# Kernel optimization log

Measured on AMD Instinct MI355X. Metric: run time of the kernel, lower is better.

Reference implementation:

```python
import jax, jax.numpy as jnp
import numpy as np
import math

V, E, N, L, S_BLOCK, R = 50257, 1024, 16, 8, 1024, 4
B, S = 2, 1024
H = E // N
IPAD = 0


def layer_norm(x, w, b, eps=1e-5):
    mu = jnp.mean(x, axis=-1, keepdims=True)
    var = jnp.mean(jnp.square(x - mu), axis=-1, keepdims=True)
    return (x - mu) * jax.lax.rsqrt(var + eps) * w + b


def setup_inputs():
    key = jax.random.key(0)
    ks = jax.random.split(key, 10)
    nrm = lambda k, shape: jax.random.normal(k, shape, jnp.float32) * 0.02
    return {
        "x": jax.random.randint(ks[0], (B, S), 1, V, dtype=jnp.int32),
        "tok_emb": nrm(ks[1], (V, E)),
        "pos_emb": nrm(ks[2], (S_BLOCK, E)),
        "dec_ln_w": jnp.ones((E,), jnp.float32),
        "dec_ln_b": jnp.zeros((E,), jnp.float32),
        "qkv_w": nrm(ks[3], (L, 3 * E, E)),
        "qkv_b": jnp.zeros((L, 3 * E), jnp.float32),
        "attn_proj_w": nrm(ks[4], (L, E, E)),
        "attn_proj_b": jnp.zeros((L, E), jnp.float32),
        "ln1_w": jnp.ones((L, E), jnp.float32),
        "ln1_b": jnp.zeros((L, E), jnp.float32),
        "fc_w": nrm(ks[5], (L, R * E, E)),
        "fc_b": jnp.zeros((L, R * E), jnp.float32),
        "mlp_proj_w": nrm(ks[6], (L, E, R * E)),
        "mlp_proj_b": jnp.zeros((L, E), jnp.float32),
        "ln2_w": jnp.ones((L, E), jnp.float32),
        "ln2_b": jnp.zeros((L, E), jnp.float32),
        "fin_ln_w": jnp.ones((E,), jnp.float32),
        "fin_ln_b": jnp.zeros((E,), jnp.float32),
    }


def _forward(x, tok_emb, pos_emb, dec_ln_w, dec_ln_b, qkv_w, qkv_b,
             attn_proj_w, attn_proj_b, ln1_w, ln1_b, fc_w, fc_b,
             mlp_proj_w, mlp_proj_b, ln2_w, ln2_b, fin_ln_w, fin_ln_b):
    # token + positional embedding
    h = tok_emb[x] + pos_emb[:S][None, :, :]  # [B,S,E]
    # attention mask: causal AND key-not-pad (ipad=0, no cache -> C=0)
    causal = jnp.tril(jnp.ones((S, S), bool))  # [S,S]
    keypad = (x != IPAD)  # [B,S]
    mask = causal[None, None, :, :] & keypad[:, None, None, :]  # [B,1,S,S]
    scale = 1.0 / math.sqrt(H)

    # Decoder: ln then dropout(eval no-op) before blocks
    h = layer_norm(h, dec_ln_w, dec_ln_b)

    def block(h, p):
        (qw, qb, pw, pb, l1w, l1b, fw, fb, mw, mb, l2w, l2b) = p
        qkv = h @ qw.T + qb  # [B,S,3E]
        q, k, v = jnp.split(qkv, 3, axis=-1)
        q = q.reshape(B, S, N, H).transpose(0, 2, 1, 3)  # [B,N,S,H]
        k = k.reshape(B, S, N, H).transpose(0, 2, 1, 3)
        v = v.reshape(B, S, N, H).transpose(0, 2, 1, 3)
        scores = jnp.einsum('bnsh,bnth->bnst', q, k) * scale  # [B,N,S,S]
        scores = jnp.where(mask, scores, -jnp.inf)
        attn = jax.nn.softmax(scores, axis=-1)
        o = jnp.einsum('bnst,bnth->bnsh', attn, v)
        o = o.transpose(0, 2, 1, 3).reshape(B, S, E)
        o = o @ pw.T + pb
        h = layer_norm(o + h, l1w, l1b)  # post-norm
        m = jax.nn.gelu(h @ fw.T + fb, approximate=False) @ mw.T + mb
        h = layer_norm(m + h, l2w, l2b)
        return h, None

    params = (qkv_w, qkv_b, attn_proj_w, attn_proj_b, ln1_w, ln1_b,
              fc_w, fc_b, mlp_proj_w, mlp_proj_b, ln2_w, ln2_b)
    h, _ = jax.lax.scan(block, h, params)
    # final Transformer LayerNorm
    return layer_norm(h, fin_ln_w, fin_ln_b)


def reference(x, tok_emb, pos_emb, dec_ln_w, dec_ln_b, qkv_w, qkv_b,
              attn_proj_w, attn_proj_b, ln1_w, ln1_b, fc_w, fc_b,
              mlp_proj_w, mlp_proj_b, ln2_w, ln2_b, fin_ln_w, fin_ln_b):
    return _forward(x, tok_emb, pos_emb, dec_ln_w, dec_ln_b, qkv_w, qkv_b,
                    attn_proj_w, attn_proj_b, ln1_w, ln1_b, fc_w, fc_b,
                    mlp_proj_w, mlp_proj_b, ln2_w, ln2_b, fin_ln_w, fin_ln_b)
```

## Files before the change

kernel.cpp:

```cpp
#include <hip/hip_runtime.h>
#include <hip/hip_bf16.h>

#define E 1024
#define SLEN 1024
#define QKV3 3072
#define HD 64

typedef unsigned short u16;
typedef unsigned int   u32;
typedef __bf16 bf16x8 __attribute__((ext_vector_type(8)));
typedef float  f32x4  __attribute__((ext_vector_type(4)));
typedef float  fv4    __attribute__((ext_vector_type(4)));
typedef u32    uv2    __attribute__((ext_vector_type(2)));

__device__ __forceinline__ u16 f2bf(float f) {
  __hip_bfloat16 h = __float2bfloat16(f);
  return __builtin_bit_cast(u16, h);
}
__device__ __forceinline__ u32 pk2(float a, float b) {
  return (u32)f2bf(a) | ((u32)f2bf(b) << 16);
}
__device__ __forceinline__ float bf2f(u32 lo16) {
  const u32 b = lo16 << 16;
  return __builtin_bit_cast(float, b);
}

__device__ __forceinline__ void gload16(const u16* g, u16* l) {
  __builtin_amdgcn_global_load_lds(
      (const __attribute__((address_space(1))) void*)g,
      (__attribute__((address_space(3))) void*)l, 16, 0, 0);
}

__device__ __forceinline__ int swzP(int row, int ch) { return (row<<4) + (ch ^ (row & 7)); }

__global__ __launch_bounds__(256)
void f2b4(const float* __restrict__ s0, u16* __restrict__ d0, int n0,
          const float* __restrict__ s1, u16* __restrict__ d1, int n1,
          const float* __restrict__ s2, u16* __restrict__ d2, int n2,
          const float* __restrict__ s3, u16* __restrict__ d3, int n3)
{
  const int total = n0 + n1 + n2 + n3;
  const int stride = gridDim.x * 256;
  for (int i = blockIdx.x * 256 + threadIdx.x; i < total; i += stride) {
    const float* s; u16* d; int j = i;
    if (j < n0) { s = s0; d = d0; }
    else if ((j -= n0) < n1) { s = s1; d = d1; }
    else if ((j -= n1) < n2) { s = s2; d = d2; }
    else { j -= n2; s = s3; d = d3; }
    const fv4 v = __builtin_nontemporal_load((const fv4*)s + j);
    uv2 o; o.x = pk2(v.x, v.y); o.y = pk2(v.z, v.w);
    ((uv2*)d)[j] = o;
  }
}

template<int BN, int OUTBF, int GELU, int SK, int SWCX, int SWCY>
__global__ __launch_bounds__(256)
void gemm_lds(const u16* __restrict__ A, const u16* __restrict__ W,
              const float* __restrict__ bias, void* __restrict__ Cv,
              int M, int N, int K)
{
  static_assert(!(GELU && SK > 1), "gelu needs full sum");
  constexpr int BM = 128;
  __shared__ __align__(16) u16 sA[3][BM*32];
  __shared__ __align__(16) u16 sB[3][BN*32];

  int bx, by, bz;
  if (SWCX > 0) {
    const int gx = gridDim.x, gy = gridDim.y;
    const int bid = blockIdx.x + gx*(blockIdx.y + gy*blockIdx.z);
    const int nchx = gx / SWCX;
    const int nchy = gy / SWCY;
    const int xcd = bid & 7;
    const int within = bid >> 3;
    const int cz  = xcd / (nchx*nchy);
    const int rem = xcd % (nchx*nchy);
    bx = (rem % nchx)*SWCX + within % SWCX;
    by = (rem / nchx)*SWCY + within / SWCX;
    bz = cz;
  } else {
    bx = blockIdx.x; by = blockIdx.y; bz = blockIdx.z;
  }

  const int t = threadIdx.x;
  const int lane = t & 63;
  const int w = t >> 6;
  const int r = lane & 15;
  const int g = lane >> 4;
  const int wr = (w >> 1) * 64;
  const int wc = (w & 1) * (BN/2);

  const int row0 = by * BM;
  const int col0 = bx * BN;
  const int k0   = (SK > 1) ? bz * (K / SK) : 0;

  constexpr int ACH = BM/16;
  constexpr int NCH = ACH + BN/16;
  constexpr int CPW = NCH/4;

  const int lrow = lane >> 2;
  const int lcol = (lane & 3) << 3;

  f32x4 acc[4][BN/32];
  #pragma unroll
  for (int i=0;i<4;i++)
    #pragma unroll
    for (int j=0;j<BN/32;j++)
      acc[i][j] = f32x4{0.f,0.f,0.f,0.f};

  const int nk = (K / SK) >> 5;

  auto stage = [&](int kt, int buf) {
    #pragma unroll
    for (int i = 0; i < CPW; ++i) {
      const int c = w*CPW + i;
      if (c < ACH) {
        const u16* gp = A + (size_t)(row0 + c*16 + lrow) * K + k0 + (kt<<5) + lcol;
        gload16(gp, &sA[buf][c*512]);
      } else {
        const int cb = c - ACH;
        const u16* gp = W + (size_t)(col0 + cb*16 + lrow) * K + k0 + (kt<<5) + lcol;
        gload16(gp, &sB[buf][cb*512]);
      }
    }
  };

  stage(0, 0);
  if (nk > 1) stage(1, 1);

  int cur = 0;
  for (int kt = 0; kt < nk; ++kt) {
    if (kt + 1 < nk) asm volatile("s_waitcnt vmcnt(4)" ::: "memory");
    else             asm volatile("s_waitcnt vmcnt(0)" ::: "memory");
    __builtin_amdgcn_s_barrier();

    if (kt + 2 < nk) stage(kt + 2, (cur + 2 >= 3) ? cur - 1 : cur + 2);

    bf16x8 af[4], bfr[BN/32];
    #pragma unroll
    for (int m=0;m<4;m++)
      af[m] = *(const bf16x8*)&sA[cur][(wr + (m<<4) + r)*32 + (g<<3)];
    #pragma unroll
    for (int n=0;n<BN/32;n++)
      bfr[n] = *(const bf16x8*)&sB[cur][(wc + (n<<4) + r)*32 + (g<<3)];
    #pragma unroll
    for (int m=0;m<4;m++)
      #pragma unroll
      for (int n=0;n<BN/32;n++)
        acc[m][n] = __builtin_amdgcn_mfma_f32_16x16x32_bf16(af[m], bfr[n], acc[m][n], 0, 0, 0);

    cur = (cur + 1 >= 3) ? 0 : cur + 1;
  }

  u16*   Cb  = (u16*)Cv   + ((SK > 1) ? (size_t)bz * M * N : 0);
  float* C32 = (float*)Cv;

  #pragma unroll
  for (int n=0;n<BN/32;n++) {
    const int col = col0 + wc + (n<<4) + r;
    const float bv = (SK == 1 || bz == 0) ? bias[col] : 0.f;
    #pragma unroll
    for (int m=0;m<4;m++) {
      const int rowb = row0 + wr + (m<<4) + (g<<2);
      #pragma unroll
      for (int q=0;q<4;q++) {
        float v = acc[m][n][q] + bv;
        if (GELU) v = 0.5f * v * (1.f + erff(v * 0.70710678118f));
        if (OUTBF) Cb[(size_t)(rowb + q) * N + col] = f2bf(v);
        else       C32[(size_t)(rowb + q) * N + col] = v;
      }
    }
  }
}

__global__ __launch_bounds__(256)
void attn_fwd(const u16* __restrict__ qkv, u16* __restrict__ o,
              float* __restrict__ opart, float* __restrict__ mpart,
              float* __restrict__ lpart)
{
  __shared__ __align__(16) u16 sK[128*64];
  __shared__ __align__(16) u16 sV[64*136];
  __shared__ __align__(16) u16 sP[4*32*128];

  const int j  = blockIdx.x;
  int qt, z, ns;
  if      (j < 3)  { qt = 7; z = j;      ns = 3; }
  else if (j < 6)  { qt = 6; z = j - 3;  ns = 3; }
  else if (j < 8)  { qt = 5; z = j - 6;  ns = 2; }
  else if (j < 10) { qt = 4; z = j - 8;  ns = 2; }
  else if (j < 12) { qt = 3; z = j - 10; ns = 2; }
  else             { qt = 14 - j; z = 0; ns = 1; }
  const int T = qt + 1, base = T / ns, rem = T % ns;
  const int kt0 = z * base + (z < rem ? z : rem);
  const int kt1 = kt0 + base + (z < rem ? 1 : 0);

  const int bn = blockIdx.y;
  const int b  = bn >> 4;
  const int hd = bn & 15;

  const int t = threadIdx.x;
  const int lane = t & 63;
  const int w = t >> 6;
  const int r = lane & 15;
  const int g = lane >> 4;

  const float SC = 0.125f * 1.44269504089f;

  bf16x8 qf[2][2];
  #pragma unroll
  for (int m=0;m<2;m++)
    #pragma unroll
    for (int kk=0;kk<2;kk++)
      qf[m][kk] = *(const bf16x8*)(qkv + (size_t)(b*SLEN + qt*128 + w*32 + (m<<4) + r) * QKV3
                                   + hd*HD + (kk<<5) + (g<<3));

  float m_run[2][4], l_run[2][4];
  f32x4 aco[2][4];
  #pragma unroll
  for (int m=0;m<2;m++) {
    #pragma unroll
    for (int q=0;q<4;q++) { m_run[m][q] = -1e30f; l_run[m][q] = 0.f; }
    #pragma unroll
    for (int n=0;n<4;n++) aco[m][n] = f32x4{0.f,0.f,0.f,0.f};
  }

  u16* sPw = sP + (w << 12);

  for (int kt = kt0; kt < kt1; ++kt) {
    __syncthreads();
    {
      const int rl = lane >> 3;
      const int hc = (lane & 7) ^ rl;
      #pragma unroll
      for (int i=0;i<4;i++) {
        const int c = w*4 + i;
        const u16* gp = qkv + (size_t)(b*SLEN + kt*128 + c*8 + rl) * QKV3
                      + E + hd*HD + (hc<<3);
        gload16(gp, &sK[c*512]);
      }
    }
    {
      const int vh = t & 63;
      const int tb = (t >> 6) << 5;
      const u16* vp = qkv + (size_t)(b*SLEN + kt*128 + tb) * QKV3 + 2*E + hd*HD + vh;
      #pragma unroll
      for (int i=0;i<32;i+=2) {
        const u32 v0 = vp[(size_t)i * QKV3];
        const u32 v1 = vp[(size_t)(i+1) * QKV3];
        const int tt = tb + i;
        const int gran = vh*17 + (tt >> 3);
        *(u32*)&sV[(gran<<3) + (tt & 7)] = v0 | (v1 << 16);
      }
    }
    __syncthreads();

    f32x4 s[2][8];
    #pragma unroll
    for (int m=0;m<2;m++)
      #pragma unroll
      for (int n=0;n<8;n++)
        s[m][n] = f32x4{0.f,0.f,0.f,0.f};
    __builtin_amdgcn_s_setprio(1);
    #pragma unroll
    for (int kk=0;kk<2;kk++) {
      bf16x8 kf[8];
      #pragma unroll
      for (int n=0;n<8;n++)
        kf[n] = *(const bf16x8*)&sK[((n<<4)+r)*64 + ((((kk<<2)+g) ^ (r&7))<<3)];
      #pragma unroll
      for (int m=0;m<2;m++)
        #pragma unroll
        for (int n=0;n<8;n++)
          s[m][n] = __builtin_amdgcn_mfma_f32_16x16x32_bf16(qf[m][kk], kf[n], s[m][n], 0,0,0);
    }
    __builtin_amdgcn_s_setprio(0);
    #pragma unroll
    for (int m=0;m<2;m++)
      #pragma unroll
      for (int n=0;n<8;n++)
        #pragma unroll
        for (int q=0;q<4;q++)
          s[m][n][q] *= SC;

    if (kt == qt) {
      #pragma unroll
      for (int m=0;m<2;m++)
        #pragma unroll
        for (int n=0;n<8;n++) {
          const int tg = (n<<4) + r;
          #pragma unroll
          for (int q=0;q<4;q++) {
            const int qg = w*32 + (m<<4) + (g<<2) + q;
            if (tg > qg) s[m][n][q] = -1e30f;
          }
        }
    }

    #pragma unroll
    for (int m=0;m<2;m++) {
      float f[4], rs[4];
      #pragma unroll
      for (int q=0;q<4;q++) {
        float v = s[m][0][q];
        #pragma unroll
        for (int n=1;n<8;n++) v = fmaxf(v, s[m][n][q]);
        v = fmaxf(v, __shfl_xor(v, 1));
        v = fmaxf(v, __shfl_xor(v, 2));
        v = fmaxf(v, __shfl_xor(v, 4));
        v = fmaxf(v, __shfl_xor(v, 8));
        const float mn = fmaxf(m_run[m][q], v);
        f[q] = exp2f(m_run[m][q] - mn);
        m_run[m][q] = mn;
        rs[q] = 0.f;
      }
      #pragma unroll
      for (int n=0;n<8;n++) {
        #pragma unroll
        for (int q=0;q<4;q++) {
          const float p = exp2f(s[m][n][q] - m_run[m][q]);
          rs[q] += p;
          const int prow = (m<<4) + (g<<2) + q;
          const int pch = (n<<1) + (r>>3);
          sPw[(swzP(prow, pch)<<3) + (r&7)] = f2bf(p);
        }
      }
      #pragma unroll
      for (int q=0;q<4;q++) {
        rs[q] += __shfl_xor(rs[q], 1);
        rs[q] += __shfl_xor(rs[q], 2);
        rs[q] += __shfl_xor(rs[q], 4);
        rs[q] += __shfl_xor(rs[q], 8);
        l_run[m][q] = l_run[m][q]*f[q] + rs[q];
      }
      #pragma unroll
      for (int n=0;n<4;n++)
        #pragma unroll
        for (int q=0;q<4;q++)
          aco[m][n][q] *= f[q];
    }

    __builtin_amdgcn_s_waitcnt(0);
    __builtin_amdgcn_sched_barrier(0);

    __builtin_amdgcn_s_setprio(1);
    #pragma unroll
    for (int kk=0;kk<4;kk++) {
      bf16x8 pf[2], vf[4];
      #pragma unroll
      for (int m=0;m<2;m++)
        pf[m] = *(const bf16x8*)&sPw[swzP((m<<4)+r, (kk<<2)+g)<<3];
      #pragma unroll
      for (int n=0;n<4;n++)
        vf[n] = *(const bf16x8*)&sV[(((n<<4)+r)*17 + (kk<<2) + g)<<3];
      #pragma unroll
      for (int m=0;m<2;m++)
        #pragma unroll
        for (int n=0;n<4;n++)
          aco[m][n] = __builtin_amdgcn_mfma_f32_16x16x32_bf16(pf[m], vf[n], aco[m][n], 0,0,0);
    }
    __builtin_amdgcn_s_setprio(0);
  }

  if (ns == 1) {
    #pragma unroll
    for (int m=0;m<2;m++)
      #pragma unroll
      for (int n=0;n<4;n++) {
        const int col = hd*HD + (n<<4) + r;
        #pragma unroll
        for (int q=0;q<4;q++) {
          const int qg = qt*128 + w*32 + (m<<4) + (g<<2) + q;
          o[(size_t)(b*SLEN + qg) * E + col] = f2bf(aco[m][n][q] / l_run[m][q]);
        }
      }
  } else {
    const size_t pb = (((size_t)z*32 + bn)*5 + (qt - 3)) * 128;
    float* op = opart + pb * 64;
    #pragma unroll
    for (int m=0;m<2;m++)
      #pragma unroll
      for (int n=0;n<4;n++) {
        #pragma unroll
        for (int q=0;q<4;q++) {
          const int row = w*32 + (m<<4) + (g<<2) + q;
          op[(size_t)row * 64 + (n<<4) + r] = aco[m][n][q];
        }
      }
    if (r == 0) {
      #pragma unroll
      for (int m=0;m<2;m++)
        #pragma unroll
        for (int q=0;q<4;q++) {
          const int row = w*32 + (m<<4) + (g<<2) + q;
          mpart[pb + row] = m_run[m][q];
          lpart[pb + row] = l_run[m][q];
        }
    }
  }
}

__global__ __launch_bounds__(256)
void attn_combine(const float* __restrict__ opart, const float* __restrict__ mpart,
                  const float* __restrict__ lpart, u16* __restrict__ o)
{
  const int qi = blockIdx.x;
  const int qt = qi + 3;
  const int np = (qt >= 6) ? 3 : 2;
  const int bn = blockIdx.y;
  const int b  = bn >> 4;
  const int hd = bn & 15;
  const int t = threadIdx.x;
  const int row = t >> 1;
  const int c0  = (t & 1) << 5;

  float4 acc[8];
  #pragma unroll
  for (int i=0;i<8;i++) acc[i] = make_float4(0.f,0.f,0.f,0.f);
  float m = -1e30f, l = 0.f;

  for (int z = 0; z < np; ++z) {
    const size_t pz = (((size_t)z*32 + bn)*5 + qi) * 128 + row;
    const float mz = mpart[pz], lz = lpart[pz];
    const float nm = fmaxf(m, mz);
    const float fo = exp2f(m - nm), fn = exp2f(mz - nm);
    const float4* oz = (const float4*)(opart + pz*64 + c0);
    #pragma unroll
    for (int i=0;i<8;i++) {
      const float4 v = oz[i];
      acc[i].x = acc[i].x*fo + v.x*fn;
      acc[i].y = acc[i].y*fo + v.y*fn;
      acc[i].z = acc[i].z*fo + v.z*fn;
      acc[i].w = acc[i].w*fo + v.w*fn;
    }
    l = l*fo + lz*fn;
    m = nm;
  }
  const float inv = 1.f / l;
  u16* ob = o + (size_t)(b*SLEN + qt*128 + row) * E + hd*HD + c0;
  #pragma unroll
  for (int i=0;i<8;i++) {
    uint2 pk; pk.x = pk2(acc[i].x*inv, acc[i].y*inv); pk.y = pk2(acc[i].z*inv, acc[i].w*inv);
    ((uint2*)ob)[i] = pk;
  }
}

__global__ __launch_bounds__(256)
void ln_bf(const u16* __restrict__ a0, const u16* __restrict__ a1,
           const u16* __restrict__ a2, const u16* __restrict__ a3,
           const u16* __restrict__ res,
           const float* __restrict__ lw, const float* __restrict__ lb,
           u16* __restrict__ outb, float* __restrict__ out32)
{
  __shared__ float red[8];
  const int row = blockIdx.x;
  const int i = threadIdx.x;
  const size_t base = (size_t)row << 10;

  uint2 pk0 = ((const uint2*)(a0 + base))[i];
  float4 v;
  v.x = bf2f(pk0.x & 0xffff); v.y = bf2f(pk0.x >> 16);
  v.z = bf2f(pk0.y & 0xffff); v.w = bf2f(pk0.y >> 16);
  auto addp = [&](const u16* a) {
    uint2 pk1 = ((const uint2*)(a + base))[i];
    v.x += bf2f(pk1.x & 0xffff); v.y += bf2f(pk1.x >> 16);
    v.z += bf2f(pk1.y & 0xffff); v.w += bf2f(pk1.y >> 16);
  };
  if (a1 != nullptr) addp(a1);
  if (a2 != nullptr) addp(a2);
  if (a3 != nullptr) addp(a3);
  if (res != nullptr) addp(res);

  float s1 = v.x + v.y + v.z + v.w;
  float s2 = v.x*v.x + v.y*v.y + v.z*v.z + v.w*v.w;
  #pragma unroll
  for (int off=1; off<64; off<<=1) { s1 += __shfl_xor(s1, off); s2 += __shfl_xor(s2, off); }
  if ((i & 63) == 0) { red[(i>>6)*2] = s1; red[(i>>6)*2+1] = s2; }
  __syncthreads();
  s1 = red[0] + red[2] + red[4] + red[6];
  s2 = red[1] + red[3] + red[5] + red[7];
  const float mean = s1 * (1.f/1024.f);
  const float var  = s2 * (1.f/1024.f) - mean*mean;
  const float rstd = rsqrtf(var + 1e-5f);
  const float4 wv = ((const float4*)lw)[i];
  const float4 bv = ((const float4*)lb)[i];
  float4 ov;
  ov.x = (v.x - mean)*rstd*wv.x + bv.x;
  ov.y = (v.y - mean)*rstd*wv.y + bv.y;
  ov.z = (v.z - mean)*rstd*wv.z + bv.z;
  ov.w = (v.w - mean)*rstd*wv.w + bv.w;
  if (outb) {
    uint2 pk; pk.x = pk2(ov.x, ov.y); pk.y = pk2(ov.z, ov.w);
    ((uint2*)(outb + base))[i] = pk;
  }
  if (out32) ((float4*)(out32 + base))[i] = ov;
}

__global__ __launch_bounds__(256)
void embed_ln(const int* __restrict__ x, const float* __restrict__ tok,
              const float* __restrict__ pos, const float* __restrict__ lw,
              const float* __restrict__ lb, u16* __restrict__ hb)
{
  __shared__ float red[8];
  const int row = blockIdx.x;
  const int s = row & (SLEN-1);
  const int i = threadIdx.x;
  const int id = x[row];
  const float4 tv = ((const float4*)(tok + ((size_t)id << 10)))[i];
  const float4 pv = ((const float4*)(pos + ((size_t)s << 10)))[i];
  float4 v;
  v.x = tv.x + pv.x; v.y = tv.y + pv.y; v.z = tv.z + pv.z; v.w = tv.w + pv.w;
  float s1 = v.x + v.y + v.z + v.w;
  float s2 = v.x*v.x + v.y*v.y + v.z*v.z + v.w*v.w;
  #pragma unroll
  for (int off=1; off<64; off<<=1) { s1 += __shfl_xor(s1, off); s2 += __shfl_xor(s2, off); }
  if ((i & 63) == 0) { red[(i>>6)*2] = s1; red[(i>>6)*2+1] = s2; }
  __syncthreads();
  s1 = red[0] + red[2] + red[4] + red[6];
  s2 = red[1] + red[3] + red[5] + red[7];
  const float mean = s1 * (1.f/1024.f);
  const float var  = s2 * (1.f/1024.f) - mean*mean;
  const float rstd = rsqrtf(var + 1e-5f);
  const float4 wv = ((const float4*)lw)[i];
  const float4 bv = ((const float4*)lb)[i];
  float4 ov;
  ov.x = (v.x - mean)*rstd*wv.x + bv.x;
  ov.y = (v.y - mean)*rstd*wv.y + bv.y;
  ov.z = (v.z - mean)*rstd*wv.z + bv.z;
  ov.w = (v.w - mean)*rstd*wv.w + bv.w;
  uint2 pk; pk.x = pk2(ov.x, ov.y); pk.y = pk2(ov.z, ov.w);
  ((uint2*)(hb + ((size_t)row << 10)))[i] = pk;
}

extern "C" void kernel_launch(void* const* d_in, const int* in_sizes, int n_in,
                              void* d_out, int out_size, void* d_ws, size_t ws_size,
                              hipStream_t stream) {
  const int*   x    = (const int*)  d_in[0];
  const float* tok  = (const float*)d_in[1];
  const float* pos  = (const float*)d_in[2];
  const float* decw = (const float*)d_in[3];
  const float* decb = (const float*)d_in[4];
  const float* qkvw = (const float*)d_in[5];
  const float* qkvb = (const float*)d_in[6];
  const float* apw  = (const float*)d_in[7];
  const float* apb  = (const float*)d_in[8];
  const float* l1w  = (const float*)d_in[9];
  const float* l1b  = (const float*)d_in[10];
  const float* fcw  = (const float*)d_in[11];
  const float* fcb  = (const float*)d_in[12];
  const float* mpw  = (const float*)d_in[13];
  const float* mpb  = (const float*)d_in[14];
  const float* l2w  = (const float*)d_in[15];
  const float* l2b  = (const float*)d_in[16];
  const float* finw = (const float*)d_in[17];
  const float* finb = (const float*)d_in[18];
  float* out = (float*)d_out;

  char* p = (char*)d_ws;
  float* opart = (float*)p;                p += (size_t)3*32*5*128*64*4;
  float* mpart = (float*)p;                p += (size_t)3*32*5*128*4;
  float* lpart = (float*)p;                p += (size_t)3*32*5*128*4;
  u16*   partb = (u16*)p;                  p += (size_t)4*2048*1024*2;
  u16*   hb    = (u16*)p;                  p += (size_t)2048*1024*2;
  u16*   qkvB  = (u16*)p;                  p += (size_t)2048*3072*2;
  u16*   ab    = (u16*)p;                  p += (size_t)2048*1024*2;
  u16*   fb    = (u16*)p;                  p += (size_t)2048*4096*2;
  u16*   wq    = (u16*)p;                  p += (size_t)8*3072*1024*2;
  u16*   wap   = (u16*)p;                  p += (size_t)8*1024*1024*2;
  u16*   wfc   = (u16*)p;                  p += (size_t)8*4096*1024*2;
  u16*   wmp   = (u16*)p;                  p += (size_t)8*4096*1024*2;
  u16*   pb1 = partb + (size_t)2048*1024;
  u16*   pb2 = partb + (size_t)2*2048*1024;
  u16*   pb3 = partb + (size_t)3*2048*1024;

  f2b4<<<4096, 256, 0, stream>>>(qkvw, wq,  8*3072*1024/4,
                                 apw,  wap, 8*1024*1024/4,
                                 fcw,  wfc, 8*4096*1024/4,
                                 mpw,  wmp, 8*4096*1024/4);

  embed_ln<<<2048, 256, 0, stream>>>(x, tok, pos, decw, decb, hb);

  for (int l = 0; l < 8; ++l) {
    const u16* lwq  = wq  + (size_t)l*3072*1024;
    const u16* lwap = wap + (size_t)l*1024*1024;
    const u16* lwfc = wfc + (size_t)l*4096*1024;
    const u16* lwmp = wmp + (size_t)l*4096*1024;

    gemm_lds<128,1,0,1,6,8><<<dim3(24,16),  256, 0, stream>>>(hb, lwq,  qkvb + (size_t)l*3072, qkvB, 2048, 3072, 1024);
    attn_fwd<<<dim3(15,32), 256, 0, stream>>>(qkvB, ab, opart, mpart, lpart);
    attn_combine<<<dim3(5,32), 256, 0, stream>>>(opart, mpart, lpart, ab);
    gemm_lds<128,1,0,4,8,8><<<dim3(8,16,4), 256, 0, stream>>>(ab, lwap, apb + (size_t)l*1024, partb, 2048, 1024, 1024);
    ln_bf<<<2048, 256, 0, stream>>>(partb, pb1, pb2, pb3, hb, l1w + (size_t)l*1024, l1b + (size_t)l*1024, hb, nullptr);
    gemm_lds<128,1,1,1,8,8><<<dim3(32,16),  256, 0, stream>>>(hb, lwfc, fcb + (size_t)l*4096, fb, 2048, 4096, 1024);
    gemm_lds<128,1,0,4,8,8><<<dim3(8,16,4), 256, 0, stream>>>(fb, lwmp, mpb + (size_t)l*1024, partb, 2048, 1024, 4096);
    ln_bf<<<2048, 256, 0, stream>>>(partb, pb1, pb2, pb3, hb, l2w + (size_t)l*1024, l2b + (size_t)l*1024, hb, nullptr);
  }

  ln_bf<<<2048, 256, 0, stream>>>(hb, nullptr, nullptr, nullptr, nullptr, finw, finb, nullptr, out);
}
```

Before: 1.275 ms.

## Split-K the QKV GEMM into two partials and sum them inside attention

The QKV projection GEMM now runs with split-K of 2, doubling its grid to 768 workgroups, and writes two bf16 partial buffers. The attention kernel loads Q, K and V from both partials and adds them during the load. K staging moves from async global_load_lds to register loads, an add, and swizzled LDS stores. The aim is better GPU occupancy for the QKV GEMM, at the cost of twice the partial-output traffic, redundant K/V re-reads and adds across query tiles, and an extra bf16 rounding step.

```diff
diff --git a/kernel.cpp b/kernel.cpp
--- a/kernel.cpp
+++ b/kernel.cpp
@@ -23,6 +23,10 @@
 __device__ __forceinline__ float bf2f(u32 lo16) {
   const u32 b = lo16 << 16;
   return __builtin_bit_cast(float, b);
+}
+__device__ __forceinline__ u32 addpk(u32 a, u32 b) {
+  return pk2(bf2f(a & 0xffff) + bf2f(b & 0xffff),
+             bf2f(a >> 16)    + bf2f(b >> 16));
 }
 
 __device__ __forceinline__ void gload16(const u16* g, u16* l) {
@@ -173,7 +177,8 @@
 }
 
 __global__ __launch_bounds__(256)
-void attn_fwd(const u16* __restrict__ qkv, u16* __restrict__ o,
+void attn_fwd(const u16* __restrict__ q0, const u16* __restrict__ q1,
+              u16* __restrict__ o,
               float* __restrict__ opart, float* __restrict__ mpart,
               float* __restrict__ lpart)
 {
@@ -209,9 +214,16 @@
   #pragma unroll
   for (int m=0;m<2;m++)
     #pragma unroll
-    for (int kk=0;kk<2;kk++)
-      qf[m][kk] = *(const bf16x8*)(qkv + (size_t)(b*SLEN + qt*128 + w*32 + (m<<4) + r) * QKV3
-                                   + hd*HD + (kk<<5) + (g<<3));
+    for (int kk=0;kk<2;kk++) {
+      const size_t off = (size_t)(b*SLEN + qt*128 + w*32 + (m<<4) + r) * QKV3
+                       + hd*HD + (kk<<5) + (g<<3);
+      const uint4 a = *(const uint4*)(q0 + off);
+      const uint4 c = *(const uint4*)(q1 + off);
+      uint4 s4;
+      s4.x = addpk(a.x, c.x); s4.y = addpk(a.y, c.y);
+      s4.z = addpk(a.z, c.z); s4.w = addpk(a.w, c.w);
+      qf[m][kk] = __builtin_bit_cast(bf16x8, s4);
+    }
 
   float m_run[2][4], l_run[2][4];
   f32x4 aco[2][4];
@@ -228,27 +240,34 @@
   for (int kt = kt0; kt < kt1; ++kt) {
     __syncthreads();
     {
-      const int rl = lane >> 3;
-      const int hc = (lane & 7) ^ rl;
+      const int krow = t >> 1;
+      const int gb = (t & 1) << 2;
+      const size_t rowoff = (size_t)(b*SLEN + kt*128 + krow) * QKV3 + E + hd*HD;
       #pragma unroll
       for (int i=0;i<4;i++) {
-        const int c = w*4 + i;
-        const u16* gp = qkv + (size_t)(b*SLEN + kt*128 + c*8 + rl) * QKV3
-                      + E + hd*HD + (hc<<3);
-        gload16(gp, &sK[c*512]);
+        const int G = gb + i;
+        const uint4 a = *(const uint4*)(q0 + rowoff + (G<<3));
+        const uint4 c = *(const uint4*)(q1 + rowoff + (G<<3));
+        uint4 s4;
+        s4.x = addpk(a.x, c.x); s4.y = addpk(a.y, c.y);
+        s4.z = addpk(a.z, c.z); s4.w = addpk(a.w, c.w);
+        const int s = G ^ (krow & 7);
+        *(uint4*)&sK[krow*64 + (s<<3)] = s4;
       }
     }
     {
       const int vh = t & 63;
       const int tb = (t >> 6) << 5;
-      const u16* vp = qkv + (size_t)(b*SLEN + kt*128 + tb) * QKV3 + 2*E + hd*HD + vh;
+      const size_t voff = (size_t)(b*SLEN + kt*128 + tb) * QKV3 + 2*E + hd*HD + vh;
+      const u16* vp0 = q0 + voff;
+      const u16* vp1 = q1 + voff;
       #pragma unroll
       for (int i=0;i<32;i+=2) {
-        const u32 v0 = vp[(size_t)i * QKV3];
-        const u32 v1 = vp[(size_t)(i+1) * QKV3];
+        const float v0 = bf2f(vp0[(size_t)i * QKV3])     + bf2f(vp1[(size_t)i * QKV3]);
+        const float v1 = bf2f(vp0[(size_t)(i+1) * QKV3]) + bf2f(vp1[(size_t)(i+1) * QKV3]);
         const int tt = tb + i;
         const int gran = vh*17 + (tt >> 3);
-        *(u32*)&sV[(gran<<3) + (tt & 7)] = v0 | (v1 << 16);
+        *(u32*)&sV[(gran<<3) + (tt & 7)] = pk2(v0, v1);
       }
     }
     __syncthreads();
@@ -560,7 +579,7 @@
   float* lpart = (float*)p;                p += (size_t)3*32*5*128*4;
   u16*   partb = (u16*)p;                  p += (size_t)4*2048*1024*2;
   u16*   hb    = (u16*)p;                  p += (size_t)2048*1024*2;
-  u16*   qkvB  = (u16*)p;                  p += (size_t)2048*3072*2;
+  u16*   qkvP  = (u16*)p;                  p += (size_t)2*2048*3072*2;
   u16*   ab    = (u16*)p;                  p += (size_t)2048*1024*2;
   u16*   fb    = (u16*)p;                  p += (size_t)2048*4096*2;
   u16*   wq    = (u16*)p;                  p += (size_t)8*3072*1024*2;
@@ -570,6 +589,7 @@
   u16*   pb1 = partb + (size_t)2048*1024;
   u16*   pb2 = partb + (size_t)2*2048*1024;
   u16*   pb3 = partb + (size_t)3*2048*1024;
+  u16*   qkvP1 = qkvP + (size_t)2048*3072;
 
   f2b4<<<4096, 256, 0, stream>>>(qkvw, wq,  8*3072*1024/4,
                                  apw,  wap, 8*1024*1024/4,
@@ -584,8 +604,8 @@
     const u16* lwfc = wfc + (size_t)l*4096*1024;
     const u16* lwmp = wmp + (size_t)l*4096*1024;
 
-    gemm_lds<128,1,0,1,6,8><<<dim3(24,16),  256, 0, stream>>>(hb, lwq,  qkvb + (size_t)l*3072, qkvB, 2048, 3072, 1024);
-    attn_fwd<<<dim3(15,32), 256, 0, stream>>>(qkvB, ab, opart, mpart, lpart);
+    gemm_lds<128,1,0,2,12,8><<<dim3(24,16,2), 256, 0, stream>>>(hb, lwq,  qkvb + (size_t)l*3072, qkvP, 2048, 3072, 1024);
+    attn_fwd<<<dim3(15,32), 256, 0, stream>>>(qkvP, qkvP1, ab, opart, mpart, lpart);
     attn_combine<<<dim3(5,32), 256, 0, stream>>>(opart, mpart, lpart, ab);
     gemm_lds<128,1,0,4,8,8><<<dim3(8,16,4), 256, 0, stream>>>(ab, lwap, apb + (size_t)l*1024, partb, 2048, 1024, 1024);
     ln_bf<<<2048, 256, 0, stream>>>(partb, pb1, pb2, pb3, hb, l1w + (size_t)l*1024, l1b + (size_t)l*1024, hb, nullptr);
```

Result: slower. 1.967 ms (+54.3%).
